# Kernel optimization log

Hardware: AMD Instinct MI355X
Metric: run time of the kernel (lower is better)

## Reference

```python
import jax, jax.numpy as jnp
import numpy as np
from math import factorial
from fractions import Fraction

MUL = 16          # multiplicity per irrep
LMAX = 2          # irreps l = 0, 1, 2
N_BATCH = 1024
RS = [(MUL, l, 0) for l in range(LMAX + 1)]   # Rs_1 = Rs_2


def _su2_cg_coeff(j1, m1, j2, m2, j3, m3):
    if m3 != m1 + m2:
        return 0.0
    f = factorial
    vmin = max(-j1 + j2 + m3, -j1 + m1, 0)
    vmax = min(j2 + j3 + m1, j3 - j1 + j2, j3 + m3)
    C = ((2 * j3 + 1) * Fraction(
        f(j3 + j1 - j2) * f(j3 - j1 + j2) * f(j1 + j2 - j3) * f(j3 + m3) * f(j3 - m3),
        f(j1 + j2 + j3 + 1) * f(j1 - m1) * f(j1 + m1) * f(j2 - m2) * f(j2 + m2))) ** 0.5
    S = 0
    for v in range(vmin, vmax + 1):
        S += (-1) ** (v + j2 + m2) * Fraction(
            f(j2 + j3 + m1 - v) * f(j1 - m1 + v),
            f(v) * f(j3 - j1 + j2 - v) * f(j3 + m3 - v) * f(v + j1 - j2 - m3))
    return float(C * S)


def _su2_cg(j1, j2, j3):
    mat = np.zeros((2 * j1 + 1, 2 * j2 + 1, 2 * j3 + 1))
    for m1 in range(-j1, j1 + 1):
        for m2 in range(-j2, j2 + 1):
            m3 = m1 + m2
            if abs(m3) <= j3:
                mat[j1 + m1, j2 + m2, j3 + m3] = _su2_cg_coeff(j1, m1, j2, m2, j3, m3)
    return mat


def _q_real_to_complex(l):
    q = np.zeros((2 * l + 1, 2 * l + 1), dtype=np.complex128)
    for m in range(-l, 0):
        q[l + m, l + abs(m)] = 2 ** -0.5
        q[l + m, l - abs(m)] = -1j * 2 ** -0.5
    q[l, l] = 1.0
    for m in range(1, l + 1):
        q[l + m, l + abs(m)] = (-1) ** m * 2 ** -0.5
        q[l + m, l - abs(m)] = 1j * (-1) ** m * 2 ** -0.5
    return (-1j) ** l * q


def _real_cg(l_out, l1, l2):
    # real-basis Wigner-3j block, shape (2*l_out+1, 2*l1+1, 2*l2+1)
    C = _su2_cg(l1, l2, l_out).astype(np.complex128)
    Q1, Q2, Q3 = _q_real_to_complex(l1), _q_real_to_complex(l2), _q_real_to_complex(l_out)
    C = np.einsum('ij,kl,mn,ikn->jlm', Q1, Q2, np.conj(Q3.T), C)
    C = np.real(C).transpose(2, 0, 1)   # -> (k, i, j)
    n = np.linalg.norm(C)
    assert n > 1e-8
    # wigner_3j has unit Frobenius norm; 'component' normalization multiplies by sqrt(2*l_out+1)
    return C / n * (2 * l_out + 1) ** 0.5


def _simplify(Rs):
    out = []
    for mul, l, p in Rs:
        if out and out[-1][1] == l and out[-1][2] == p:
            out[-1][0] += mul
        elif mul > 0:
            out.append([mul, l, p])
    return out


def _sort_dst(Rs):
    # stable sort of irrep blocks by (l, p); returns dst[old_row] = new_row
    xs, j = [], 0
    for mul, l, p in Rs:
        d = mul * (2 * l + 1)
        xs.append((l, p, mul, j, d))
        j += d
    dst = np.zeros(j, dtype=np.int64)
    i = 0
    for l, p, mul, jo, d in sorted(xs):
        dst[jo:jo + d] = np.arange(i, i + d)
        i += d
    return dst


def _build_sparse_tp(Rs1, Rs2):
    # replicates _tensor_product_in_in with the default selection rule
    rows, iis, jjs, vs = [], [], [], []
    Rs_out = []
    index_out = 0
    index_1 = 0
    for mul1, l1, p1 in Rs1:
        index_2 = 0
        for mul2, l2, p2 in Rs2:
            for l_out in range(abs(l1 - l2), l1 + l2 + 1):
                C = _real_cg(l_out, l1, l2)
                kc, ic, jc = np.nonzero(np.abs(C) > 1e-12)
                cv = C[kc, ic, jc]
                w = np.arange(mul1 * mul2)
                u, v = w // mul2, w % mul2
                rows.append((index_out + w[:, None] * (2 * l_out + 1) + kc[None, :]).ravel())
                iis.append((index_1 + u[:, None] * (2 * l1 + 1) + ic[None, :]).ravel())
                jjs.append((index_2 + v[:, None] * (2 * l2 + 1) + jc[None, :]).ravel())
                vs.append(np.tile(cv, mul1 * mul2))
                Rs_out.append([mul1 * mul2, l_out, p1 * p2])
                index_out += mul1 * mul2 * (2 * l_out + 1)
            index_2 += mul2 * (2 * l2 + 1)
        index_1 += mul1 * (2 * l1 + 1)
    k_idx = np.concatenate(rows)
    dst = _sort_dst(_simplify(Rs_out))   # sorted=True in the original module
    k_idx = dst[k_idx]
    return (k_idx, np.concatenate(iis), np.concatenate(jjs),
            np.concatenate(vs).astype(np.float32), index_out)


def setup_inputs() -> dict:
    key = jax.random.key(0)
    k1, k2 = jax.random.split(key)
    k_idx, i_idx, j_idx, vals, dim_out = _build_sparse_tp(RS, RS)
    dim_in = sum(mul * (2 * l + 1) for mul, l, _ in RS)   # 144
    x1 = jax.random.normal(k1, (N_BATCH, dim_in), dtype=jnp.float32)
    x2 = jax.random.normal(k2, (N_BATCH, dim_in), dtype=jnp.float32)
    return {"x1": x1, "x2": x2,
            "vals": jnp.asarray(vals),
            "k_idx": jnp.asarray(k_idx),
            "i_idx": jnp.asarray(i_idx),
            "j_idx": jnp.asarray(j_idx),
            "dim_out": int(dim_out)}


def reference(x1, x2, vals, k_idx, i_idx, j_idx, dim_out):
    # out[z, k] = sum_{nnz with row k} vals * x1[z, i] * x2[z, j]
    # (sparse Wigner-3j tensor contracted with the outer product of the inputs)
    prod = x1[:, i_idx] * x2[:, j_idx] * vals[None, :]               # [N, nnz]
    out = jax.ops.segment_sum(prod.T, k_idx, num_segments=dim_out)   # [dim_out, N]
    return out.T
```

## Files before the change

kernel.cpp:

```cpp
#include <hip/hip_runtime.h>


#define ZPT 32
#define BLK 512
#define DIM_IN 144
#define STRIDE 36

__global__ void prep_kernel(const int* __restrict__ k_idx,
                            const float* __restrict__ vals,
                            const int* __restrict__ i_idx,
                            const int* __restrict__ j_idx,
                            int nnz,
                            int* __restrict__ seg_start,
                            int* __restrict__ seg_end,
                            int2* __restrict__ packed) {
    int n = blockIdx.x * blockDim.x + threadIdx.x;
    if (n >= nnz) return;
    int k = k_idx[n];
    if (n == 0 || k_idx[n - 1] != k) seg_start[k] = n;
    if (n == nnz - 1 || k_idx[n + 1] != k) seg_end[k] = n + 1;
    packed[n] = make_int2(i_idx[n] | (j_idx[n] << 16), __float_as_int(vals[n]));
}

__global__ __launch_bounds__(BLK) void tp_kernel(
        const float* __restrict__ x1,
        const float* __restrict__ x2,
        const int2* __restrict__ packed,
        const int* __restrict__ seg_start,
        const int* __restrict__ seg_end,
        float* __restrict__ out,
        int dim_out) {
    __shared__ __align__(16) float x1s[DIM_IN * STRIDE];
    __shared__ __align__(16) float x2s[DIM_IN * STRIDE];

    const int z0 = blockIdx.y * ZPT;
    const int k  = blockIdx.x * BLK + threadIdx.x;

    int s = 0, e = 0;
    if (k < dim_out) {
        s = seg_start[k];
        e = seg_end[k];
    }

    for (int idx = threadIdx.x; idx < ZPT * (DIM_IN / 4); idx += BLK) {
        const int t  = idx / (DIM_IN / 4);
        const int i4 = idx % (DIM_IN / 4);
        const float4 a = *(const float4*)(x1 + (size_t)(z0 + t) * DIM_IN + i4 * 4);
        const float4 b = *(const float4*)(x2 + (size_t)(z0 + t) * DIM_IN + i4 * 4);
        const int base = i4 * 4 * STRIDE + t;
        x1s[base             ] = a.x;
        x1s[base +     STRIDE] = a.y;
        x1s[base + 2 * STRIDE] = a.z;
        x1s[base + 3 * STRIDE] = a.w;
        x2s[base             ] = b.x;
        x2s[base +     STRIDE] = b.y;
        x2s[base + 2 * STRIDE] = b.z;
        x2s[base + 3 * STRIDE] = b.w;
    }
    __syncthreads();

    if (k >= dim_out) return;

    float acc[ZPT];
#pragma unroll
    for (int t = 0; t < ZPT; ++t) acc[t] = 0.0f;

    int n = s;
    if (n < e) {
        int2 ev = packed[n];
        for (;;) {
            const bool more = (n + 1 < e);
            int2 evn;
            if (more) evn = packed[n + 1];

            const float c = __int_as_float(ev.y);
            const int i = ev.x & 0xffff;
            const int j = ev.x >> 16;
            const float4* p1 = (const float4*)(x1s + i * STRIDE);
            const float4* p2 = (const float4*)(x2s + j * STRIDE);
#pragma unroll
            for (int q = 0; q < ZPT / 4; ++q) {
                const float4 a = p1[q];
                const float4 b = p2[q];
                acc[4 * q + 0] += c * a.x * b.x;
                acc[4 * q + 1] += c * a.y * b.y;
                acc[4 * q + 2] += c * a.z * b.z;
                acc[4 * q + 3] += c * a.w * b.w;
            }

            ++n;
            if (!more) break;
            ev = evn;
        }
    }

#pragma unroll
    for (int t = 0; t < ZPT; ++t) {
        out[(size_t)(z0 + t) * dim_out + k] = acc[t];
    }
}

extern "C" void kernel_launch(void* const* d_in, const int* in_sizes, int n_in,
                              void* d_out, int out_size, void* d_ws, size_t ws_size,
                              hipStream_t stream) {
    const float* x1   = (const float*)d_in[0];
    const float* x2   = (const float*)d_in[1];
    const float* vals = (const float*)d_in[2];
    const int*   kidx = (const int*)d_in[3];
    const int*   iidx = (const int*)d_in[4];
    const int*   jidx = (const int*)d_in[5];
    float* out = (float*)d_out;

    const int n_batch = 1024;
    const int dim_out = out_size / n_batch;
    const int nnz     = in_sizes[2];

    int*  seg_start = (int*)d_ws;
    int*  seg_end   = seg_start + dim_out;
    int2* packed    = (int2*)(seg_end + dim_out);

    {
        int grid = (nnz + 255) / 256;
        prep_kernel<<<grid, 256, 0, stream>>>(kidx, vals, iidx, jidx, nnz,
                                              seg_start, seg_end, packed);
    }

    {
        dim3 grid((dim_out + BLK - 1) / BLK, 1024 / ZPT);
        tp_kernel<<<grid, BLK, 0, stream>>>(x1, x2, packed,
                                            seg_start, seg_end, out, dim_out);
    }
}
```

Before: 31.81 us.

## Loop persistent blocks over batch groups with double-buffered shared tiles

Each block now walks several 16-row batch groups in a grid-stride loop instead of handling one 32-row group, and alternates between two shared-memory buffers so the next group's stage can start while slower threads finish the previous one. Segment bounds are loaded once per block and reused across groups, and the smaller per-thread accumulator lowers register pressure. The cost is a much smaller grid (16 in y), which gives less parallelism for hiding latency. There is also only one barrier per iteration: a thread can overwrite a buffer two iterations later while slower threads are still reading it, which is a potential race.

```diff
diff --git a/kernel.cpp b/kernel.cpp
--- a/kernel.cpp
+++ b/kernel.cpp
@@ -1,10 +1,12 @@
 #include <hip/hip_runtime.h>
 
 
-#define ZPT 32
+#define ZPT 16
 #define BLK 512
 #define DIM_IN 144
-#define STRIDE 36
+#define STRIDE 20
+#define NZG 64
+#define GRID_Y 16
 
 __global__ void prep_kernel(const int* __restrict__ k_idx,
                             const float* __restrict__ vals,
@@ -30,73 +32,82 @@
         const int* __restrict__ seg_end,
         float* __restrict__ out,
         int dim_out) {
-    __shared__ __align__(16) float x1s[DIM_IN * STRIDE];
-    __shared__ __align__(16) float x2s[DIM_IN * STRIDE];
+    __shared__ __align__(16) float x1s[2][DIM_IN * STRIDE];
+    __shared__ __align__(16) float x2s[2][DIM_IN * STRIDE];
 
-    const int z0 = blockIdx.y * ZPT;
-    const int k  = blockIdx.x * BLK + threadIdx.x;
+    const int k = blockIdx.x * BLK + threadIdx.x;
+    const bool live = (k < dim_out);
 
     int s = 0, e = 0;
-    if (k < dim_out) {
+    if (live) {
         s = seg_start[k];
         e = seg_end[k];
     }
 
-    for (int idx = threadIdx.x; idx < ZPT * (DIM_IN / 4); idx += BLK) {
-        const int t  = idx / (DIM_IN / 4);
-        const int i4 = idx % (DIM_IN / 4);
-        const float4 a = *(const float4*)(x1 + (size_t)(z0 + t) * DIM_IN + i4 * 4);
-        const float4 b = *(const float4*)(x2 + (size_t)(z0 + t) * DIM_IN + i4 * 4);
-        const int base = i4 * 4 * STRIDE + t;
-        x1s[base             ] = a.x;
-        x1s[base +     STRIDE] = a.y;
-        x1s[base + 2 * STRIDE] = a.z;
-        x1s[base + 3 * STRIDE] = a.w;
-        x2s[base             ] = b.x;
-        x2s[base +     STRIDE] = b.y;
-        x2s[base + 2 * STRIDE] = b.z;
-        x2s[base + 3 * STRIDE] = b.w;
-    }
-    __syncthreads();
+    int p = 0;
+    for (int g = blockIdx.y; g < NZG; g += GRID_Y, p ^= 1) {
+        const int z0 = g * ZPT;
 
-    if (k >= dim_out) return;
+        for (int idx = threadIdx.x; idx < ZPT * (DIM_IN / 4); idx += BLK) {
+            const int t  = idx / (DIM_IN / 4);
+            const int i4 = idx % (DIM_IN / 4);
+            const float4 a = *(const float4*)(x1 + (size_t)(z0 + t) * DIM_IN + i4 * 4);
+            const float4 b = *(const float4*)(x2 + (size_t)(z0 + t) * DIM_IN + i4 * 4);
+            const int base = i4 * 4 * STRIDE + t;
+            float* d1 = x1s[p];
+            float* d2 = x2s[p];
+            d1[base             ] = a.x;
+            d1[base +     STRIDE] = a.y;
+            d1[base + 2 * STRIDE] = a.z;
+            d1[base + 3 * STRIDE] = a.w;
+            d2[base             ] = b.x;
+            d2[base +     STRIDE] = b.y;
+            d2[base + 2 * STRIDE] = b.z;
+            d2[base + 3 * STRIDE] = b.w;
+        }
+        __syncthreads();
 
-    float acc[ZPT];
+        if (live) {
+            float acc[ZPT];
 #pragma unroll
-    for (int t = 0; t < ZPT; ++t) acc[t] = 0.0f;
+            for (int t = 0; t < ZPT; ++t) acc[t] = 0.0f;
 
-    int n = s;
-    if (n < e) {
-        int2 ev = packed[n];
-        for (;;) {
-            const bool more = (n + 1 < e);
-            int2 evn;
-            if (more) evn = packed[n + 1];
+            int n = s;
+            if (n < e) {
+                int2 ev = packed[n];
+                const float* b1 = x1s[p];
+                const float* b2 = x2s[p];
+                for (;;) {
+                    const bool more = (n + 1 < e);
+                    int2 evn;
+                    if (more) evn = packed[n + 1];
 
-            const float c = __int_as_float(ev.y);
-            const int i = ev.x & 0xffff;
-            const int j = ev.x >> 16;
-            const float4* p1 = (const float4*)(x1s + i * STRIDE);
-            const float4* p2 = (const float4*)(x2s + j * STRIDE);
+                    const float c = __int_as_float(ev.y);
+                    const int i = ev.x & 0xffff;
+                    const int j = ev.x >> 16;
+                    const float4* p1 = (const float4*)(b1 + i * STRIDE);
+                    const float4* p2 = (const float4*)(b2 + j * STRIDE);
 #pragma unroll
-            for (int q = 0; q < ZPT / 4; ++q) {
-                const float4 a = p1[q];
-                const float4 b = p2[q];
-                acc[4 * q + 0] += c * a.x * b.x;
-                acc[4 * q + 1] += c * a.y * b.y;
-                acc[4 * q + 2] += c * a.z * b.z;
-                acc[4 * q + 3] += c * a.w * b.w;
+                    for (int q = 0; q < ZPT / 4; ++q) {
+                        const float4 a = p1[q];
+                        const float4 b = p2[q];
+                        acc[4 * q + 0] += c * a.x * b.x;
+                        acc[4 * q + 1] += c * a.y * b.y;
+                        acc[4 * q + 2] += c * a.z * b.z;
+                        acc[4 * q + 3] += c * a.w * b.w;
+                    }
+
+                    ++n;
+                    if (!more) break;
+                    ev = evn;
+                }
             }
 
-            ++n;
-            if (!more) break;
-            ev = evn;
+#pragma unroll
+            for (int t = 0; t < ZPT; ++t) {
+                out[(size_t)(z0 + t) * dim_out + k] = acc[t];
+            }
         }
-    }
-
-#pragma unroll
-    for (int t = 0; t < ZPT; ++t) {
-        out[(size_t)(z0 + t) * dim_out + k] = acc[t];
     }
 }
 
@@ -126,7 +137,7 @@
     }
 
     {
-        dim3 grid((dim_out + BLK - 1) / BLK, 1024 / ZPT);
+        dim3 grid((dim_out + BLK - 1) / BLK, GRID_Y);
         tp_kernel<<<grid, BLK, 0, stream>>>(x1, x2, packed,
                                             seg_start, seg_end, out, dim_out);
     }
```

After: 34.62 us. 1.09x slower.

## Halve batch tile, issue global loads early, and loop nnz per 4-row chunk

Applied to the files above, without the earlier changes.

Halves the batch rows per block from 32 to 16, which doubles the grid and shrinks shared memory through a smaller stride. Each thread's global loads for staging x1/x2 are now issued before the segment bounds are read, so the two latencies overlap. The accumulation is restructured so each thread walks its nnz segment once per 4-row chunk with only 4 accumulators. This cuts register pressure to raise occupancy, at the cost of re-reading the packed index list several times per thread.

```diff
diff --git a/kernel.cpp b/kernel.cpp
--- a/kernel.cpp
+++ b/kernel.cpp
@@ -1,10 +1,10 @@
 #include <hip/hip_runtime.h>
 
 
-#define ZPT 32
+#define ZPT 16
 #define BLK 512
 #define DIM_IN 144
-#define STRIDE 36
+#define STRIDE 20
 
 __global__ void prep_kernel(const int* __restrict__ k_idx,
                             const float* __restrict__ vals,
@@ -35,68 +35,94 @@
 
     const int z0 = blockIdx.y * ZPT;
     const int k  = blockIdx.x * BLK + threadIdx.x;
+    const bool live = (k < dim_out);
+
+    const int n4 = ZPT * (DIM_IN / 4);
+    const int s0 = threadIdx.x;
+    const int s1 = threadIdx.x + BLK;
+    float4 a0, b0, a1, b1;
+    {
+        const int t  = s0 / (DIM_IN / 4);
+        const int i4 = s0 % (DIM_IN / 4);
+        a0 = *(const float4*)(x1 + (size_t)(z0 + t) * DIM_IN + i4 * 4);
+        b0 = *(const float4*)(x2 + (size_t)(z0 + t) * DIM_IN + i4 * 4);
+    }
+    if (s1 < n4) {
+        const int t  = s1 / (DIM_IN / 4);
+        const int i4 = s1 % (DIM_IN / 4);
+        a1 = *(const float4*)(x1 + (size_t)(z0 + t) * DIM_IN + i4 * 4);
+        b1 = *(const float4*)(x2 + (size_t)(z0 + t) * DIM_IN + i4 * 4);
+    }
 
     int s = 0, e = 0;
-    if (k < dim_out) {
+    if (live) {
         s = seg_start[k];
         e = seg_end[k];
     }
 
-    for (int idx = threadIdx.x; idx < ZPT * (DIM_IN / 4); idx += BLK) {
-        const int t  = idx / (DIM_IN / 4);
-        const int i4 = idx % (DIM_IN / 4);
-        const float4 a = *(const float4*)(x1 + (size_t)(z0 + t) * DIM_IN + i4 * 4);
-        const float4 b = *(const float4*)(x2 + (size_t)(z0 + t) * DIM_IN + i4 * 4);
+    {
+        const int t  = s0 / (DIM_IN / 4);
+        const int i4 = s0 % (DIM_IN / 4);
         const int base = i4 * 4 * STRIDE + t;
-        x1s[base             ] = a.x;
-        x1s[base +     STRIDE] = a.y;
-        x1s[base + 2 * STRIDE] = a.z;
-        x1s[base + 3 * STRIDE] = a.w;
-        x2s[base             ] = b.x;
-        x2s[base +     STRIDE] = b.y;
-        x2s[base + 2 * STRIDE] = b.z;
-        x2s[base + 3 * STRIDE] = b.w;
+        x1s[base             ] = a0.x;
+        x1s[base +     STRIDE] = a0.y;
+        x1s[base + 2 * STRIDE] = a0.z;
+        x1s[base + 3 * STRIDE] = a0.w;
+        x2s[base             ] = b0.x;
+        x2s[base +     STRIDE] = b0.y;
+        x2s[base + 2 * STRIDE] = b0.z;
+        x2s[base + 3 * STRIDE] = b0.w;
+    }
+    if (s1 < n4) {
+        const int t  = s1 / (DIM_IN / 4);
+        const int i4 = s1 % (DIM_IN / 4);
+        const int base = i4 * 4 * STRIDE + t;
+        x1s[base             ] = a1.x;
+        x1s[base +     STRIDE] = a1.y;
+        x1s[base + 2 * STRIDE] = a1.z;
+        x1s[base + 3 * STRIDE] = a1.w;
+        x2s[base             ] = b1.x;
+        x2s[base +     STRIDE] = b1.y;
+        x2s[base + 2 * STRIDE] = b1.z;
+        x2s[base + 3 * STRIDE] = b1.w;
     }
     __syncthreads();
 
-    if (k >= dim_out) return;
-
-    float acc[ZPT];
-#pragma unroll
-    for (int t = 0; t < ZPT; ++t) acc[t] = 0.0f;
-
-    int n = s;
-    if (n < e) {
-        int2 ev = packed[n];
-        for (;;) {
-            const bool more = (n + 1 < e);
-            int2 evn;
-            if (more) evn = packed[n + 1];
-
-            const float c = __int_as_float(ev.y);
-            const int i = ev.x & 0xffff;
-            const int j = ev.x >> 16;
-            const float4* p1 = (const float4*)(x1s + i * STRIDE);
-            const float4* p2 = (const float4*)(x2s + j * STRIDE);
-#pragma unroll
-            for (int q = 0; q < ZPT / 4; ++q) {
-                const float4 a = p1[q];
-                const float4 b = p2[q];
-                acc[4 * q + 0] += c * a.x * b.x;
-                acc[4 * q + 1] += c * a.y * b.y;
-                acc[4 * q + 2] += c * a.z * b.z;
-                acc[4 * q + 3] += c * a.w * b.w;
-            }
-
-            ++n;
-            if (!more) break;
-            ev = evn;
-        }
-    }
+    if (!live) return;
 
 #pragma unroll
-    for (int t = 0; t < ZPT; ++t) {
-        out[(size_t)(z0 + t) * dim_out + k] = acc[t];
+    for (int q = 0; q < ZPT / 4; ++q) {
+        float ac0 = 0.0f, ac1 = 0.0f, ac2 = 0.0f, ac3 = 0.0f;
+
+        int n = s;
+        if (n < e) {
+            int2 ev = packed[n];
+            for (;;) {
+                const bool more = (n + 1 < e);
+                int2 evn;
+                if (more) evn = packed[n + 1];
+
+                const float c = __int_as_float(ev.y);
+                const int i = ev.x & 0xffff;
+                const int j = ev.x >> 16;
+                const float4 a = *(const float4*)(x1s + i * STRIDE + 4 * q);
+                const float4 b = *(const float4*)(x2s + j * STRIDE + 4 * q);
+                ac0 += c * a.x * b.x;
+                ac1 += c * a.y * b.y;
+                ac2 += c * a.z * b.z;
+                ac3 += c * a.w * b.w;
+
+                ++n;
+                if (!more) break;
+                ev = evn;
+            }
+        }
+
+        float* o = out + (size_t)(z0 + 4 * q) * dim_out + k;
+        o[0]                    = ac0;
+        o[(size_t)dim_out]      = ac1;
+        o[(size_t)2 * dim_out]  = ac2;
+        o[(size_t)3 * dim_out]  = ac3;
     }
 }
 
```

Result: slower. 38.27 us (+20.3%).

## Process batch in small generations with register-prefetched next tile

Applied to the files above, without the earlier changes.

Shrinks the per-thread batch tile from 32 to 8 rows and the block from 512 to 256 threads. Each block now loops over four generations of 8 batch rows, prefetching the next generation's inputs into registers while the current one computes, then writing them to LDS between barriers. The aim is lower register pressure and higher occupancy, and hiding global load latency behind compute. In exchange, the sparse index stream is re-read once per generation and extra barriers are added.

```diff
diff --git a/kernel.cpp b/kernel.cpp
--- a/kernel.cpp
+++ b/kernel.cpp
@@ -1,10 +1,14 @@
 #include <hip/hip_runtime.h>
 
 
-#define ZPT 32
-#define BLK 512
+#define ZPT 8
+#define BLK 256
 #define DIM_IN 144
-#define STRIDE 36
+#define NQ (DIM_IN / 4)
+#define N4 (ZPT * NQ)
+#define STRIDE 12
+#define GENS 4
+#define GRID_Y 32
 
 __global__ void prep_kernel(const int* __restrict__ k_idx,
                             const float* __restrict__ vals,
@@ -22,6 +26,15 @@
     packed[n] = make_int2(i_idx[n] | (j_idx[n] << 16), __float_as_int(vals[n]));
 }
 
+__device__ __forceinline__ void lds_write_t(float* dst, int i4, int t,
+                                            const float4& v) {
+    const int base = i4 * 4 * STRIDE + t;
+    dst[base             ] = v.x;
+    dst[base +     STRIDE] = v.y;
+    dst[base + 2 * STRIDE] = v.z;
+    dst[base + 3 * STRIDE] = v.w;
+}
+
 __global__ __launch_bounds__(BLK) void tp_kernel(
         const float* __restrict__ x1,
         const float* __restrict__ x2,
@@ -33,70 +46,107 @@
     __shared__ __align__(16) float x1s[DIM_IN * STRIDE];
     __shared__ __align__(16) float x2s[DIM_IN * STRIDE];
 
-    const int z0 = blockIdx.y * ZPT;
-    const int k  = blockIdx.x * BLK + threadIdx.x;
+    const int tid = threadIdx.x;
+    const int k   = blockIdx.x * BLK + tid;
+    const bool live = (k < dim_out);
 
     int s = 0, e = 0;
-    if (k < dim_out) {
+    if (live) {
         s = seg_start[k];
         e = seg_end[k];
     }
 
-    for (int idx = threadIdx.x; idx < ZPT * (DIM_IN / 4); idx += BLK) {
-        const int t  = idx / (DIM_IN / 4);
-        const int i4 = idx % (DIM_IN / 4);
-        const float4 a = *(const float4*)(x1 + (size_t)(z0 + t) * DIM_IN + i4 * 4);
-        const float4 b = *(const float4*)(x2 + (size_t)(z0 + t) * DIM_IN + i4 * 4);
-        const int base = i4 * 4 * STRIDE + t;
-        x1s[base             ] = a.x;
-        x1s[base +     STRIDE] = a.y;
-        x1s[base + 2 * STRIDE] = a.z;
-        x1s[base + 3 * STRIDE] = a.w;
-        x2s[base             ] = b.x;
-        x2s[base +     STRIDE] = b.y;
-        x2s[base + 2 * STRIDE] = b.z;
-        x2s[base + 3 * STRIDE] = b.w;
+    const int t0 = tid / NQ,        i40 = tid % NQ;
+    const int t1 = (tid + BLK) / NQ, i41 = (tid + BLK) % NQ;
+    const bool has1 = (tid + BLK) < N4;
+
+    const int zg0 = blockIdx.y * GENS;
+
+    {
+        const int z0 = zg0 * ZPT;
+        float4 A0 = *(const float4*)(x1 + (size_t)(z0 + t0) * DIM_IN + i40 * 4);
+        float4 B0 = *(const float4*)(x2 + (size_t)(z0 + t0) * DIM_IN + i40 * 4);
+        float4 A1, B1;
+        if (has1) {
+            A1 = *(const float4*)(x1 + (size_t)(z0 + t1) * DIM_IN + i41 * 4);
+            B1 = *(const float4*)(x2 + (size_t)(z0 + t1) * DIM_IN + i41 * 4);
+        }
+        lds_write_t(x1s, i40, t0, A0);
+        lds_write_t(x2s, i40, t0, B0);
+        if (has1) {
+            lds_write_t(x1s, i41, t1, A1);
+            lds_write_t(x2s, i41, t1, B1);
+        }
     }
     __syncthreads();
 
-    if (k >= dim_out) return;
+#pragma unroll
+    for (int gen = 0; gen < GENS; ++gen) {
+        const int z0 = (zg0 + gen) * ZPT;
+        const bool more_gen = (gen + 1 < GENS);
 
-    float acc[ZPT];
+        float4 nA0, nB0, nA1, nB1;
+        if (more_gen) {
+            const int nz0 = z0 + ZPT;
+            nA0 = *(const float4*)(x1 + (size_t)(nz0 + t0) * DIM_IN + i40 * 4);
+            nB0 = *(const float4*)(x2 + (size_t)(nz0 + t0) * DIM_IN + i40 * 4);
+            if (has1) {
+                nA1 = *(const float4*)(x1 + (size_t)(nz0 + t1) * DIM_IN + i41 * 4);
+                nB1 = *(const float4*)(x2 + (size_t)(nz0 + t1) * DIM_IN + i41 * 4);
+            }
+        }
+
+        float acc[ZPT];
 #pragma unroll
-    for (int t = 0; t < ZPT; ++t) acc[t] = 0.0f;
+        for (int t = 0; t < ZPT; ++t) acc[t] = 0.0f;
 
-    int n = s;
-    if (n < e) {
-        int2 ev = packed[n];
-        for (;;) {
-            const bool more = (n + 1 < e);
-            int2 evn;
-            if (more) evn = packed[n + 1];
+        if (live) {
+            int n = s;
+            if (n < e) {
+                int2 ev = packed[n];
+                for (;;) {
+                    const bool more = (n + 1 < e);
+                    int2 evn;
+                    if (more) evn = packed[n + 1];
 
-            const float c = __int_as_float(ev.y);
-            const int i = ev.x & 0xffff;
-            const int j = ev.x >> 16;
-            const float4* p1 = (const float4*)(x1s + i * STRIDE);
-            const float4* p2 = (const float4*)(x2s + j * STRIDE);
+                    const float c = __int_as_float(ev.y);
+                    const int i = ev.x & 0xffff;
+                    const int j = ev.x >> 16;
+                    const float4* p1 = (const float4*)(x1s + i * STRIDE);
+                    const float4* p2 = (const float4*)(x2s + j * STRIDE);
 #pragma unroll
-            for (int q = 0; q < ZPT / 4; ++q) {
-                const float4 a = p1[q];
-                const float4 b = p2[q];
-                acc[4 * q + 0] += c * a.x * b.x;
-                acc[4 * q + 1] += c * a.y * b.y;
-                acc[4 * q + 2] += c * a.z * b.z;
-                acc[4 * q + 3] += c * a.w * b.w;
+                    for (int q = 0; q < ZPT / 4; ++q) {
+                        const float4 a = p1[q];
+                        const float4 b = p2[q];
+                        acc[4 * q + 0] += c * a.x * b.x;
+                        acc[4 * q + 1] += c * a.y * b.y;
+                        acc[4 * q + 2] += c * a.z * b.z;
+                        acc[4 * q + 3] += c * a.w * b.w;
+                    }
+
+                    ++n;
+                    if (!more) break;
+                    ev = evn;
+                }
             }
 
-            ++n;
-            if (!more) break;
-            ev = evn;
+#pragma unroll
+            for (int t = 0; t < ZPT; ++t) {
+                out[(size_t)(z0 + t) * dim_out + k] = acc[t];
+            }
         }
-    }
 
-#pragma unroll
-    for (int t = 0; t < ZPT; ++t) {
-        out[(size_t)(z0 + t) * dim_out + k] = acc[t];
+        __syncthreads();
+
+        if (more_gen) {
+            lds_write_t(x1s, i40, t0, nA0);
+            lds_write_t(x2s, i40, t0, nB0);
+            if (has1) {
+                lds_write_t(x1s, i41, t1, nA1);
+                lds_write_t(x2s, i41, t1, nB1);
+            }
+            __syncthreads();
+        }
     }
 }
 
@@ -126,7 +176,7 @@
     }
 
     {
-        dim3 grid((dim_out + BLK - 1) / BLK, 1024 / ZPT);
+        dim3 grid((dim_out + BLK - 1) / BLK, GRID_Y);
         tp_kernel<<<grid, BLK, 0, stream>>>(x1, x2, packed,
                                             seg_start, seg_end, out, dim_out);
     }
```

New measurement: 41.26 us. +29.7%, slower.
